# Performance work log

Hardware: AMD Instinct MI355X
Metric: run time of the kernel (lower is better)

Reference implementation:

```python
import jax, jax.numpy as jnp
import numpy as np

T, W, H = 3072, 2048, 1024   # tokens, words, hidden
C, S = 32, 3                 # labels, score channels (start/end/inside)
HID = 512                    # scorer MLP hidden
MAXW = 12                    # max span width
THR = 0.5                    # extraction threshold
N = W * MAXW                 # fixed number of enumerated spans


def setup_inputs() -> dict:
    key = jax.random.key(0)
    ks = jax.random.split(key, 16)
    hidden_states = jax.random.normal(ks[0], (T, H), jnp.float32) * 0.05
    # each word's first subword carries word_id+1; other tokens carry 0
    first_pos = (jnp.arange(W) * T // W).astype(jnp.int32)
    words_mask = jnp.zeros((T,), jnp.int32).at[first_pos].set(jnp.arange(1, W + 1, dtype=jnp.int32))
    labels_embeds = jax.random.normal(ks[1], (C, H), jnp.float32) * 0.05
    p = lambda k, shp: jax.random.normal(k, shp, jnp.float32) * 0.02
    return dict(
        hidden_states=hidden_states,
        words_mask=words_mask,
        labels_embeds=labels_embeds,
        Wt=p(ks[2], (H, 2 * H)), bt=jnp.zeros((2 * H,), jnp.float32),
        Wl=p(ks[3], (H, 2 * H)), bl=jnp.zeros((2 * H,), jnp.float32),
        W1a=p(ks[4], (H, HID)), W1b=p(ks[5], (H, HID)), W1c=p(ks[6], (H, HID)),
        b1=jnp.zeros((HID,), jnp.float32),
        W2=p(ks[7], (HID, S)), b2=jnp.zeros((S,), jnp.float32),
        Wsp1=p(ks[8], (2 * H, H)), bsp1=jnp.zeros((H,), jnp.float32),
        Wsp2=p(ks[9], (H, H)), bsp2=jnp.zeros((H,), jnp.float32),
    )


def reference(hidden_states, words_mask, labels_embeds,
              Wt, bt, Wl, bl, W1a, W1b, W1c, b1, W2, b2,
              Wsp1, bsp1, Wsp2, bsp2):
    # --- scatter token embeddings into word slots (dummy slot W absorbs mask==0) ---
    idx = jnp.where(words_mask > 0, words_mask - 1, W)
    we = jnp.zeros((W + 1, H), hidden_states.dtype).at[idx].add(hidden_states)[:W]  # [W,H]

    # --- scorer: proj to (2,H) halves, pairwise features, MLP -> [W,C,S] ---
    tok = (we @ Wt + bt).reshape(W, 2, H)
    lab = (labels_embeds @ Wl + bl).reshape(C, 2, H)
    t0, t1 = tok[:, 0], tok[:, 1]
    l0, l1 = lab[:, 0], lab[:, 1]
    # first MLP layer on concat([t0, l0, t1*l1]) computed as split matmuls
    h = (t0 @ W1a)[:, None, :] + (l0 @ W1b)[None, :, :] \
        + jnp.einsum('wh,ch,hd->wcd', t1, l1, W1c)
    h = jax.nn.relu(h + b1)
    scores = h @ W2 + b2  # [W,C,S]

    # --- threshold span extraction (fixed-shape enumeration of widths < MAXW) ---
    probs = jax.nn.sigmoid(scores)
    is_start = jnp.any(probs[..., 0] >= THR, axis=1)  # [W]
    is_end = jnp.any(probs[..., 1] >= THR, axis=1)    # [W]
    starts = jnp.repeat(jnp.arange(W), MAXW)          # [N]
    ends_raw = starts + jnp.tile(jnp.arange(MAXW), W)
    valid = ends_raw < W
    ends = jnp.minimum(ends_raw, W - 1)
    span_mask = valid & is_start[starts] & is_end[ends]  # [N]
    span_idx = jnp.stack([starts, ends], axis=-1)        # [N,2] int

    # --- span_rep_layer: gather start/end word embeds, 2-layer projection ---
    idxm = span_idx * span_mask[:, None].astype(span_idx.dtype)
    sp = jnp.concatenate([we[idxm[:, 0]], we[idxm[:, 1]]], axis=-1)  # [N,2H]
    span_rep = jax.nn.relu(sp @ Wsp1 + bsp1) @ Wsp2 + bsp2           # [N,H]

    # einsum 'BND,BCD->BNC' with B=1
    span_logits = span_rep @ labels_embeds.T  # [N,C]

    # pack_shape_prefixed_tensor equivalent: flat float payload
    flat = jnp.concatenate([
        scores.ravel(),
        span_idx.astype(scores.dtype).ravel(),
        span_mask.astype(scores.dtype),
        span_logits.ravel(),
    ])
    return flat
```

## Files before the change

kernel.cpp:

```cpp
#include <hip/hip_runtime.h>
#include <hip/hip_bf16.h>

#define W_WORDS 2048
#define H_DIM   1024
#define C_LAB   32
#define HID_D   512
#define MAXW    12
#define NSPAN   (W_WORDS * MAXW)

typedef __attribute__((ext_vector_type(8))) short bf16x8;
typedef __attribute__((ext_vector_type(4))) float f32x4;
typedef __attribute__((ext_vector_type(4))) int i32x4;
typedef __attribute__((ext_vector_type(8))) int i32x8;

__device__ __forceinline__ unsigned short f2b(float x) {
  union { float f; unsigned int i; } v; v.f = x;
  unsigned int r = v.i + 0x7FFFu + ((v.i >> 16) & 1u);
  return (unsigned short)(r >> 16);
}
__device__ __forceinline__ float b2f(unsigned short b) {
  union { float f; unsigned int i; } v; v.i = ((unsigned int)b) << 16;
  return v.f;
}

__device__ __forceinline__ unsigned char f2e4m3(float x) {
  union { float f; unsigned u; } v; v.f = x;
  unsigned sign = (v.u >> 31) << 7;
  v.u &= 0x7FFFFFFFu;
  if (v.f > 448.f) v.f = 448.f;
  int e8 = (int)(v.u >> 23) - 120;
  unsigned r;
  if (e8 >= 1) {
    unsigned m = v.u & 0x7FFFFFu;
    unsigned keep = m >> 20;
    unsigned rest = m & 0xFFFFFu;
    keep += (rest > 0x80000u) || (rest == 0x80000u && (keep & 1u));
    if (keep == 8u) { keep = 0u; ++e8; }
    if (e8 >= 16) { e8 = 15; keep = 6u; }
    else if (e8 == 15 && keep == 7u) keep = 6u;
    r = (unsigned)((e8 << 3) | keep);
  } else {
    int m = (int)(v.f * 512.f + 0.5f);
    r = (m >= 8) ? 0x08u : (unsigned)m;
  }
  return (unsigned char)(r | sign);
}

#define GLOAD_LDS16(g, l)                                                    \
  __builtin_amdgcn_global_load_lds(                                          \
      (const __attribute__((address_space(1))) unsigned int*)(g),            \
      (__attribute__((address_space(3))) unsigned int*)(l), 16, 0, 0)

__global__ void mega0_k(const float* __restrict__ hs, const int* __restrict__ wm,
    unsigned char* __restrict__ we8,
    const float* __restrict__ Wt, const float* __restrict__ W1a,
    const float* __restrict__ Wsp1, const float* __restrict__ W1c,
    const float* __restrict__ Wsp2,
    unsigned char* __restrict__ WtT8, unsigned short* __restrict__ W1aT,
    unsigned char* __restrict__ Wsp1Tc8, float* __restrict__ W1cT,
    float* __restrict__ Wsp2T, unsigned short* __restrict__ Wtb0) {
  if (blockIdx.z == 6) {
    int t = blockIdx.y * 96 + blockIdx.x;
    int m = wm[t];
    if (m <= 0) return;
    const float* src = hs + (size_t)t * H_DIM;
    unsigned char* dst = we8 + (size_t)(m - 1) * H_DIM;
    int i = (threadIdx.y * 32 + threadIdx.x) * 4;
    float4 v = *(const float4*)(src + i);
    unsigned u = (unsigned)f2e4m3(v.x * 16.f)
               | ((unsigned)f2e4m3(v.y * 16.f) << 8)
               | ((unsigned)f2e4m3(v.z * 16.f) << 16)
               | ((unsigned)f2e4m3(v.w * 16.f) << 24);
    *(unsigned*)(dst + i) = u;
    return;
  }
  int c0 = blockIdx.x * 32, r0 = blockIdx.y * 32;
  if (blockIdx.z == 7) {
    if (c0 >= 1024) return;
    for (int i = threadIdx.y; i < 32; i += 8)
      Wtb0[(size_t)(r0 + i) * 1024 + c0 + threadIdx.x] =
          f2b(Wt[(size_t)(r0 + i) * 2048 + c0 + threadIdx.x]);
    return;
  }
  const float* in;
  void* out;
  int R, C, ld, mode;
  switch (blockIdx.z) {
    case 0: in = Wt + 1024; out = WtT8; R = 1024; C = 1024; ld = 2048; mode = 2; break;
    case 1: in = W1a;  out = W1aT;   R = 1024; C = 512;  ld = 512;  mode = 1; break;
    case 2: in = Wsp1; out = Wsp1Tc8; R = 1024; C = 1024; ld = 1024; mode = 2; break;
    case 3: in = Wsp1 + 1048576; out = Wsp1Tc8 + 1048576; R = 1024; C = 1024; ld = 1024; mode = 2; break;
    case 4: in = W1c;  out = W1cT;   R = 1024; C = 512;  ld = 512;  mode = 0; break;
    default: in = Wsp2; out = Wsp2T; R = 1024; C = 1024; ld = 1024; mode = 0; break;
  }
  if (c0 >= C || r0 >= R) return;
  __shared__ float tile[32][33];
  for (int i = threadIdx.y; i < 32; i += 8)
    tile[i][threadIdx.x] = in[(size_t)(r0 + i) * ld + c0 + threadIdx.x];
  __syncthreads();
  if (mode == 2) {
    unsigned char* o = (unsigned char*)out;
    for (int i = threadIdx.y; i < 32; i += 8)
      o[(size_t)(c0 + i) * R + r0 + threadIdx.x] = f2e4m3(tile[threadIdx.x][i] * 64.f);
  } else if (mode == 1) {
    unsigned short* o = (unsigned short*)out;
    for (int i = threadIdx.y; i < 32; i += 8)
      o[(size_t)(c0 + i) * R + r0 + threadIdx.x] = f2b(tile[threadIdx.x][i]);
  } else {
    float* o = (float*)out;
    for (int i = threadIdx.y; i < 32; i += 8)
      o[(size_t)(c0 + i) * R + r0 + threadIdx.x] = tile[threadIdx.x][i];
  }
}

__device__ __forceinline__ void rgemm8_body(int N, int M,
    const float* __restrict__ A, int lda, const float* __restrict__ B, int ldb,
    const float* __restrict__ bias, float* __restrict__ out, int ldc,
    int bx, int by, float* shf) {
  float (*Asm)[1024] = (float(*)[1024])shf;
  float (*red)[16][8] = (float(*)[16][8])(shf + 8192);
  int m0 = by * 8;
  for (int idx = threadIdx.x; idx < 8 * 1024; idx += 256) {
    int mm = idx >> 10, kk = idx & 1023;
    Asm[mm][kk] = (m0 + mm < M) ? A[(size_t)(m0 + mm) * lda + kk] : 0.f;
  }
  __syncthreads();
  int tx = threadIdx.x & 15, ty = threadIdx.x >> 4;
  int n = bx * 16 + tx;
  float acc[8] = {0.f, 0.f, 0.f, 0.f, 0.f, 0.f, 0.f, 0.f};
  if (n < N) {
    for (int k = ty * 64; k < ty * 64 + 64; ++k) {
      float bv = B[(size_t)k * ldb + n];
#pragma unroll
      for (int mm = 0; mm < 8; ++mm) acc[mm] = fmaf(Asm[mm][k], bv, acc[mm]);
    }
  }
#pragma unroll
  for (int mm = 0; mm < 8; ++mm) red[ty][tx][mm] = acc[mm];
  __syncthreads();
  if (ty < 8 && n < N && m0 + ty < M) {
    float s = 0.f;
#pragma unroll
    for (int q = 0; q < 16; ++q) s += red[q][tx][ty];
    if (bias) s += bias[n];
    out[(size_t)(m0 + ty) * ldc + n] = s;
  }
}

__global__ __launch_bounds__(256) void rgemm8z_k(
    const float* __restrict__ L, const float* __restrict__ Wl,
    const float* __restrict__ bl, float* __restrict__ lab,
    const float* __restrict__ Wsp2T, float* __restrict__ MmTf) {
  __shared__ float shf[10240];
  if (blockIdx.z == 0) {
    rgemm8_body(2048, 32, L, 1024, Wl, 2048, bl, lab, 2048, blockIdx.x, blockIdx.y, shf);
  } else {
    if (blockIdx.x >= 64) return;
    rgemm8_body(1024, 32, L, 1024, Wsp2T, 1024, nullptr, MmTf, 1024,
                blockIdx.x, blockIdx.y, shf);
  }
}

__global__ __launch_bounds__(256) void mega1_k(
    const float* __restrict__ lab, const float* __restrict__ W1cT,
    unsigned char* __restrict__ KT8,
    const float* __restrict__ W1b, const float* __restrict__ b1,
    float* __restrict__ BvecB,
    const float* __restrict__ bsp2, const float* __restrict__ L,
    float* __restrict__ cv, const float* __restrict__ MmTf,
    unsigned short* __restrict__ MmTb, const float* __restrict__ W2,
    unsigned short* __restrict__ W2padT, const float* __restrict__ bsp1,
    unsigned short* __restrict__ bsp1b,
    const float* __restrict__ bt, const float* __restrict__ W1a,
    float* __restrict__ bt0A) {
  __shared__ float shf[10240];
  int g = blockIdx.x;
  if (g < 8192) {
    size_t gid = (size_t)g * 256 + threadIdx.x;
    int row = (int)(gid >> 7);
    int h0 = ((int)gid & 127) * 8;
    int c = row >> 9, d = row & 511;
    const float* lp = lab + (size_t)c * 2048 + 1024 + h0;
    const float* wp = W1cT + (size_t)d * 1024 + h0;
    float4 l0 = *(const float4*)lp, l1 = *(const float4*)(lp + 4);
    float4 w0 = *(const float4*)wp, w1 = *(const float4*)(wp + 4);
    unsigned u0 = (unsigned)f2e4m3(l0.x * w0.x * 1024.f)
                | ((unsigned)f2e4m3(l0.y * w0.y * 1024.f) << 8)
                | ((unsigned)f2e4m3(l0.z * w0.z * 1024.f) << 16)
                | ((unsigned)f2e4m3(l0.w * w0.w * 1024.f) << 24);
    unsigned u1 = (unsigned)f2e4m3(l1.x * w1.x * 1024.f)
                | ((unsigned)f2e4m3(l1.y * w1.y * 1024.f) << 8)
                | ((unsigned)f2e4m3(l1.z * w1.z * 1024.f) << 16)
                | ((unsigned)f2e4m3(l1.w * w1.w * 1024.f) << 24);
    *(uint2*)(KT8 + (size_t)row * 1024 + h0) = make_uint2(u0, u1);
  } else if (g < 8320) {
    int b = g - 8192;
    rgemm8_body(512, 32, lab, 2048, W1b, 512, b1, BvecB, 512, b & 31, b >> 5, shf);
  } else {
    int b = g - 8320;
    if (b < 32) {
      int c = b;
      float a = 0.f;
      for (int k = threadIdx.x; k < 1024; k += 256)
        a = fmaf(bsp2[k], L[(size_t)c * 1024 + k], a);
#pragma unroll
      for (int off = 32; off; off >>= 1) a += __shfl_down(a, off);
      if ((threadIdx.x & 63) == 0) shf[threadIdx.x >> 6] = a;
      __syncthreads();
      if (threadIdx.x == 0) cv[c] = shf[0] + shf[1] + shf[2] + shf[3];
    } else if (b < 64) {
      int i = (b - 32) * 1024 + threadIdx.x * 4;
      float4 v = *(const float4*)(MmTf + i);
      *(ushort4*)(MmTb + i) = make_ushort4(f2b(v.x), f2b(v.y), f2b(v.z), f2b(v.w));
    } else if (b < 96) {
      int i = (b - 64) * 256 + threadIdx.x;
      int n = i >> 9, d = i & 511;
      W2padT[i] = f2b(n < 3 ? W2[d * 3 + n] : 0.f);
    } else if (b == 96) {
      int i = threadIdx.x * 4;
      float4 v = *(const float4*)(bsp1 + i);
      *(ushort4*)(bsp1b + i) = make_ushort4(f2b(v.x), f2b(v.y), f2b(v.z), f2b(v.w));
    } else {
      float (*red)[16] = (float(*)[16])shf;
      int tx = threadIdx.x & 15, ty = threadIdx.x >> 4;
      int d = (b - 97) * 16 + tx;
      float a = 0.f;
      for (int k = ty * 64; k < ty * 64 + 64; ++k)
        a = fmaf(bt[k], W1a[(size_t)k * 512 + d], a);
      red[ty][tx] = a;
      __syncthreads();
      if (ty == 0) {
        float s = 0.f;
#pragma unroll
        for (int q = 0; q < 16; ++q) s += red[q][tx];
        bt0A[d] = s;
      }
    }
  }
}

__global__ __launch_bounds__(256) void wfuse_k(
    const unsigned short* __restrict__ A, const unsigned short* __restrict__ BT,
    unsigned char* __restrict__ out8) {
  __shared__ __align__(16) unsigned short smem[2][16384];
  int tid = threadIdx.x;
  int lane = tid & 63, wid = tid >> 6;
  int wr = wid >> 1, wc = wid & 1;
  int row0 = blockIdx.y * 128, col0 = blockIdx.x * 128;
  f32x4 zero4 = {0.f, 0.f, 0.f, 0.f};
  f32x4 acc[4][4];
#pragma unroll
  for (int i = 0; i < 4; ++i)
#pragma unroll
    for (int j = 0; j < 4; ++j) acc[i][j] = zero4;
  int srow = tid >> 3;
  int scol = ((tid & 7) ^ (srow & 7)) * 8;
  const unsigned short* gA = A + (size_t)(row0 + srow) * 1024 + scol;
  const unsigned short* gB = BT + (size_t)(col0 + srow) * 1024 + scol;
  int fr = lane & 15, hi = lane >> 4;
#define W_STAGE(buf, kt)                                                     \
  {                                                                          \
    unsigned short* dA = smem[buf] + tid * 8;                                \
    unsigned short* dB = smem[buf] + 8192 + tid * 8;                         \
    _Pragma("unroll")                                                        \
    for (int i2 = 0; i2 < 4; ++i2) {                                         \
      GLOAD_LDS16(gA + (size_t)(i2 * 32) * 1024 + (kt), dA + i2 * 2048);     \
      GLOAD_LDS16(gB + (size_t)(i2 * 32) * 1024 + (kt), dB + i2 * 2048);     \
    }                                                                        \
  }
  W_STAGE(0, 0);
  for (int t = 0; t < 16; ++t) {
    if (t + 1 < 16) {
      W_STAGE((t + 1) & 1, (t + 1) << 6);
      asm volatile("s_waitcnt vmcnt(8)" ::: "memory");
    } else {
      asm volatile("s_waitcnt vmcnt(0)" ::: "memory");
    }
    __builtin_amdgcn_sched_barrier(0);
    __builtin_amdgcn_s_barrier();
    __builtin_amdgcn_sched_barrier(0);
    const unsigned short* As = smem[t & 1];
    const unsigned short* Bs = smem[t & 1] + 8192;
    bf16x8 af[4][2], bfr[4][2];
#pragma unroll
    for (int mi = 0; mi < 4; ++mi) {
      int rl = wr * 64 + mi * 16 + fr;
#pragma unroll
      for (int kk = 0; kk < 2; ++kk)
        af[mi][kk] = *(const bf16x8*)&As[rl * 64 + (((kk << 2) | hi) ^ (rl & 7)) * 8];
    }
#pragma unroll
    for (int ni = 0; ni < 4; ++ni) {
      int rl = wc * 64 + ni * 16 + fr;
#pragma unroll
      for (int kk = 0; kk < 2; ++kk)
        bfr[ni][kk] = *(const bf16x8*)&Bs[rl * 64 + (((kk << 2) | hi) ^ (rl & 7)) * 8];
    }
#pragma unroll
    for (int kk = 0; kk < 2; ++kk)
#pragma unroll
      for (int mi = 0; mi < 4; ++mi)
#pragma unroll
        for (int ni = 0; ni < 4; ++ni)
          acc[mi][ni] = __builtin_amdgcn_mfma_f32_16x16x32_bf16(af[mi][kk], bfr[ni][kk],
                                                                acc[mi][ni], 0, 0, 0);
    __builtin_amdgcn_sched_barrier(0);
    __builtin_amdgcn_s_barrier();
  }
#undef W_STAGE
  int rbase = row0 + wr * 64 + (hi << 2);
  int cbase = col0 + wc * 64 + fr;
#pragma unroll
  for (int mi = 0; mi < 4; ++mi)
#pragma unroll
    for (int ni = 0; ni < 4; ++ni) {
      int ccol = cbase + ni * 16;
#pragma unroll
      for (int j = 0; j < 4; ++j) {
        int r = rbase + mi * 16 + j;
        out8[(size_t)r * 1024 + ccol] = f2e4m3(acc[mi][ni][j] * 64.f);
      }
    }
}

__global__ __launch_bounds__(256) void fgemm_k(
    const unsigned char* __restrict__ A, const unsigned char* __restrict__ BT,
    float* __restrict__ Avec, unsigned char* __restrict__ t1f8,
    unsigned short* __restrict__ UVb,
    const float* __restrict__ bt, const float* __restrict__ bt0A) {
  __shared__ __align__(16) unsigned char smem[2][32768];
  int tid = threadIdx.x;
  int lane = tid & 63, wid = tid >> 6;
  int wr = wid >> 1, wc = wid & 1;
  int row0 = blockIdx.y * 128, col0 = blockIdx.x * 128;
  f32x4 zero4 = {0.f, 0.f, 0.f, 0.f};
  f32x4 acc[4][4];
#pragma unroll
  for (int i = 0; i < 4; ++i)
#pragma unroll
    for (int j = 0; j < 4; ++j) acc[i][j] = zero4;
  int srow = tid >> 3;
  int s2 = (tid & 7) ^ (srow & 7);
  int scolB = (((s2 << 1) | (s2 >> 2)) & 7) * 16;
  const unsigned char* gA = A + (size_t)(row0 + srow) * 1024 + scolB;
  const unsigned char* gB = BT + (size_t)(col0 + srow) * 1024 + scolB;
  int fr = lane & 15, hi = lane >> 4;
#define F_STAGE(buf, ktB)                                                    \
  {                                                                          \
    unsigned char* dA = smem[buf] + tid * 16;                                \
    unsigned char* dB = smem[buf] + 16384 + tid * 16;                        \
    _Pragma("unroll")                                                        \
    for (int i2 = 0; i2 < 4; ++i2) {                                         \
      GLOAD_LDS16(gA + (size_t)(i2 * 32) * 1024 + (ktB), dA + i2 * 4096);    \
      GLOAD_LDS16(gB + (size_t)(i2 * 32) * 1024 + (ktB), dB + i2 * 4096);    \
    }                                                                        \
  }
  F_STAGE(0, 0);
  for (int t = 0; t < 8; ++t) {
    if (t + 1 < 8) {
      F_STAGE((t + 1) & 1, (t + 1) * 128);
      asm volatile("s_waitcnt vmcnt(8)" ::: "memory");
    } else {
      asm volatile("s_waitcnt vmcnt(0)" ::: "memory");
    }
    __builtin_amdgcn_sched_barrier(0);
    __builtin_amdgcn_s_barrier();
    __builtin_amdgcn_sched_barrier(0);
    const unsigned char* As = smem[t & 1];
    const unsigned char* Bs = smem[t & 1] + 16384;
    i32x8 af[4], bfr[4];
#pragma unroll
    for (int mi = 0; mi < 4; ++mi) {
      int rl = wr * 64 + mi * 16 + fr;
      i32x4 lo = *(const i32x4*)&As[rl * 128 + ((hi ^ (rl & 7)) * 16)];
      i32x4 h2 = *(const i32x4*)&As[rl * 128 + (((4 + hi) ^ (rl & 7)) * 16)];
      af[mi][0] = lo[0]; af[mi][1] = lo[1]; af[mi][2] = lo[2]; af[mi][3] = lo[3];
      af[mi][4] = h2[0]; af[mi][5] = h2[1]; af[mi][6] = h2[2]; af[mi][7] = h2[3];
    }
#pragma unroll
    for (int ni = 0; ni < 4; ++ni) {
      int rl = wc * 64 + ni * 16 + fr;
      i32x4 lo = *(const i32x4*)&Bs[rl * 128 + ((hi ^ (rl & 7)) * 16)];
      i32x4 h2 = *(const i32x4*)&Bs[rl * 128 + (((4 + hi) ^ (rl & 7)) * 16)];
      bfr[ni][0] = lo[0]; bfr[ni][1] = lo[1]; bfr[ni][2] = lo[2]; bfr[ni][3] = lo[3];
      bfr[ni][4] = h2[0]; bfr[ni][5] = h2[1]; bfr[ni][6] = h2[2]; bfr[ni][7] = h2[3];
    }
#pragma unroll
    for (int mi = 0; mi < 4; ++mi)
#pragma unroll
      for (int ni = 0; ni < 4; ++ni)
        acc[mi][ni] = __builtin_amdgcn_mfma_scale_f32_16x16x128_f8f6f4(
            af[mi], bfr[ni], acc[mi][ni], 0, 0, 0, 127u, 0, 127u);
    __builtin_amdgcn_sched_barrier(0);
    __builtin_amdgcn_s_barrier();
  }
#undef F_STAGE
  const float inv = 0.0009765625f;
  int rbase = row0 + wr * 64 + (hi << 2);
  int cbase = col0 + wc * 64 + fr;
#pragma unroll
  for (int mi = 0; mi < 4; ++mi)
#pragma unroll
    for (int ni = 0; ni < 4; ++ni) {
      int ccol = cbase + ni * 16;
#pragma unroll
      for (int j = 0; j < 4; ++j) {
        int r = rbase + mi * 16 + j;
        float v = acc[mi][ni][j] * inv;
        if (ccol < 1024) {
          t1f8[(size_t)r * 1024 + ccol] = f2e4m3((v + bt[1024 + ccol]) * 16.f);
        } else if (ccol < 3072) {
          UVb[(size_t)r * 2048 + (ccol - 1024)] = f2b(v);
        } else {
          Avec[(size_t)r * 512 + (ccol - 3072)] = v + bt0A[ccol - 3072];
        }
      }
    }
}

__global__ __launch_bounds__(256) void egemm_k(
    const unsigned char* __restrict__ A,
    const unsigned char* __restrict__ BT,
    const float* __restrict__ avec, const float* __restrict__ bvec,
    const unsigned short* __restrict__ w2t, float* __restrict__ sPart) {
  __shared__ __align__(16) unsigned char smem[2][32768];
  int tid = threadIdx.x;
  int lane = tid & 63, wid = tid >> 6;
  int wr = wid >> 1, wc = wid & 1;
  int bid = blockIdx.x;
  int xcd = bid & 7, ii = bid >> 3;
  int sg = ii >> 6, inner = ii & 63;
  int rb = ((sg >> 1) << 3) | (inner & 7);
  int cb = xcd * 16 + (((sg & 1) << 3) | (inner >> 3));
  int row0 = rb * 128, col0 = cb * 128, cbq = cb & 3;

  f32x4 zero4 = {0.f, 0.f, 0.f, 0.f};
  f32x4 acc[4][4];
#pragma unroll
  for (int i = 0; i < 4; ++i)
#pragma unroll
    for (int j = 0; j < 4; ++j) acc[i][j] = zero4;

  int srow = tid >> 3;
  int s2 = (tid & 7) ^ (srow & 7);
  int scolB = (((s2 << 1) | (s2 >> 2)) & 7) * 16;
  const unsigned char* gA = A + (size_t)(row0 + srow) * 1024 + scolB;
  const unsigned char* gB = BT + (size_t)(col0 + srow) * 1024 + scolB;

  int fr = lane & 15, hi = lane >> 4;

#define E_STAGE(buf, ktB)                                                    \
  {                                                                          \
    unsigned char* dA = smem[buf] + tid * 16;                                \
    unsigned char* dB = smem[buf] + 16384 + tid * 16;                        \
    _Pragma("unroll")                                                        \
    for (int i2 = 0; i2 < 4; ++i2) {                                         \
      GLOAD_LDS16(gA + (size_t)(i2 * 32) * 1024 + (ktB), dA + i2 * 4096);    \
      GLOAD_LDS16(gB + (size_t)(i2 * 32) * 1024 + (ktB), dB + i2 * 4096);    \
    }                                                                        \
  }

  E_STAGE(0, 0);

  for (int t = 0; t < 8; ++t) {
    if (t + 1 < 8) {
      E_STAGE((t + 1) & 1, (t + 1) * 128);
      asm volatile("s_waitcnt vmcnt(8)" ::: "memory");
    } else {
      asm volatile("s_waitcnt vmcnt(0)" ::: "memory");
    }
    __builtin_amdgcn_sched_barrier(0);
    __builtin_amdgcn_s_barrier();
    __builtin_amdgcn_sched_barrier(0);

    const unsigned char* As = smem[t & 1];
    const unsigned char* Bs = smem[t & 1] + 16384;
    i32x8 af[4], bfr[4];
#pragma unroll
    for (int mi = 0; mi < 4; ++mi) {
      int rl = wr * 64 + mi * 16 + fr;
      i32x4 lo = *(const i32x4*)&As[rl * 128 + ((hi ^ (rl & 7)) * 16)];
      i32x4 h2 = *(const i32x4*)&As[rl * 128 + (((4 + hi) ^ (rl & 7)) * 16)];
      af[mi][0] = lo[0]; af[mi][1] = lo[1]; af[mi][2] = lo[2]; af[mi][3] = lo[3];
      af[mi][4] = h2[0]; af[mi][5] = h2[1]; af[mi][6] = h2[2]; af[mi][7] = h2[3];
    }
#pragma unroll
    for (int ni = 0; ni < 4; ++ni) {
      int rl = wc * 64 + ni * 16 + fr;
      i32x4 lo = *(const i32x4*)&Bs[rl * 128 + ((hi ^ (rl & 7)) * 16)];
      i32x4 h2 = *(const i32x4*)&Bs[rl * 128 + (((4 + hi) ^ (rl & 7)) * 16)];
      bfr[ni][0] = lo[0]; bfr[ni][1] = lo[1]; bfr[ni][2] = lo[2]; bfr[ni][3] = lo[3];
      bfr[ni][4] = h2[0]; bfr[ni][5] = h2[1]; bfr[ni][6] = h2[2]; bfr[ni][7] = h2[3];
    }
#pragma unroll
    for (int mi = 0; mi < 4; ++mi)
#pragma unroll
      for (int ni = 0; ni < 4; ++ni)
        acc[mi][ni] = __builtin_amdgcn_mfma_scale_f32_16x16x128_f8f6f4(
            af[mi], bfr[ni], acc[mi][ni], 0, 0, 0, 127u, 0, 127u);
    __builtin_amdgcn_sched_barrier(0);
    __builtin_amdgcn_s_barrier();
  }
#undef E_STAGE

  unsigned short* hsm = (unsigned short*)&smem[0][0];
  int cc = col0 >> 9;
  int dg0 = col0 & 511;
  const float inv = 6.103515625e-05f;
#pragma unroll
  for (int mi = 0; mi < 4; ++mi) {
#pragma unroll
    for (int j = 0; j < 4; ++j) {
      int rl = wr * 64 + hi * 4 + mi * 16 + j;
      const float* avp = avec + (size_t)(row0 + rl) * 512 + dg0;
      const float* bvp = bvec + (size_t)cc * 512 + dg0;
#pragma unroll
      for (int ni = 0; ni < 4; ++ni) {
        int cl = wc * 64 + ni * 16 + fr;
        float v = acc[mi][ni][j] * inv + avp[cl] + bvp[cl];
        v = fmaxf(v, 0.f);
        int slot = cl >> 3;
        hsm[rl * 128 + (((slot ^ rl) & 7) << 3) + (slot & 8) * 8 + (cl & 7)] = f2b(v);
      }
    }
  }
  __syncthreads();
  f32x4 s0 = zero4, s1 = zero4;
  int r0l = wid * 32 + fr;
  int r1l = wid * 32 + 16 + fr;
#pragma unroll
  for (int kt2 = 0; kt2 < 4; ++kt2) {
    int slot = kt2 * 4 + hi;
    bf16x8 a0 = *(const bf16x8*)&hsm[r0l * 128 + (((slot ^ r0l) & 7) << 3) + (slot & 8) * 8];
    bf16x8 a1 = *(const bf16x8*)&hsm[r1l * 128 + (((slot ^ r1l) & 7) << 3) + (slot & 8) * 8];
    bf16x8 b = *(const bf16x8*)&w2t[(size_t)fr * 512 + dg0 + kt2 * 32 + hi * 8];
    s0 = __builtin_amdgcn_mfma_f32_16x16x32_bf16(a0, b, s0, 0, 0, 0);
    s1 = __builtin_amdgcn_mfma_f32_16x16x32_bf16(a1, b, s1, 0, 0, 0);
  }
  if (fr < 3) {
    float* sp = sPart + ((size_t)cbq * 2048 + row0) * 96 + cc * 3 + fr;
#pragma unroll
    for (int j = 0; j < 4; ++j) {
      sp[(size_t)(wid * 32 + hi * 4 + j) * 96] = s0[j];
      sp[(size_t)(wid * 32 + 16 + hi * 4 + j) * 96] = s1[j];
    }
  }
}

__global__ __launch_bounds__(256) void foldmask_k(const float* __restrict__ part,
    const float* __restrict__ b2, float* __restrict__ outS,
    int* __restrict__ is_s, int* __restrict__ is_e) {
  __shared__ float sc[192];
  int b = blockIdx.x;
  int i = threadIdx.x;
  if (i < 192) {
    int idx = b * 192 + i;
    float s = b2[i % 3] + part[idx] + part[196608 + idx] +
              part[2 * 196608 + idx] + part[3 * 196608 + idx];
    outS[idx] = s;
    sc[i] = s;
  }
  __syncthreads();
  if (i < 2) {
    int s = 0, e = 0;
#pragma unroll
    for (int c = 0; c < 32; ++c) {
      s |= (sc[i * 96 + c * 3 + 0] >= 0.f);
      e |= (sc[i * 96 + c * 3 + 1] >= 0.f);
    }
    is_s[2 * b + i] = s;
    is_e[2 * b + i] = e;
  }
}

__global__ __launch_bounds__(256) void spanfuse_k(
    const unsigned short* __restrict__ UVb, const unsigned short* __restrict__ bsp1b,
    const unsigned short* __restrict__ MmTb, const float* __restrict__ cvv,
    const int* __restrict__ is_s, const int* __restrict__ is_e,
    float* __restrict__ outIdx, float* __restrict__ outMask,
    float* __restrict__ outLog) {
  __shared__ __align__(16) unsigned short Rs[4][2][16][32];
  int tid = threadIdx.x, lane = tid & 63, w = tid >> 6;
  int fr = lane & 15, hi = lane >> 4;
  int row = lane >> 2, q = lane & 3;
  int n = blockIdx.x * 64 + w * 16 + row;
  int wi = n / MAXW;
  int j = n - wi * MAXW;
  int er = wi + j;
  int valid = er < W_WORDS;
  int e = valid ? er : (W_WORDS - 1);
  int mask = (valid && is_s[wi] && is_e[e]) ? 1 : 0;
  if (q == 0) {
    outIdx[2 * n] = (float)wi;
    outIdx[2 * n + 1] = (float)e;
    outMask[n] = (float)mask;
  }
  int si = mask ? wi : 0, ei = mask ? e : 0;
  const unsigned short* Up = UVb + (size_t)si * 2048 + q * 8;
  const unsigned short* Vp = UVb + (size_t)ei * 2048 + 1024 + q * 8;
  const unsigned short* bp = bsp1b + q * 8;
  const unsigned short* M0 = MmTb + (size_t)fr * 1024 + hi * 8;
  const unsigned short* M1 = MmTb + (size_t)(16 + fr) * 1024 + hi * 8;
  unsigned short* wRs0 = &Rs[w][0][0][0];
  unsigned short* wRs1 = &Rs[w][1][0][0];
  int wslot = (q ^ (row & 3)) * 8;
  int rslot = ((hi ^ (fr & 3)) & 3) * 8;
  f32x4 zero4 = {0.f, 0.f, 0.f, 0.f};
  f32x4 a0 = zero4, a1 = zero4;

  bf16x8 u0 = *(const bf16x8*)Up,        v0 = *(const bf16x8*)Vp;
  bf16x8 b0 = *(const bf16x8*)bp;
  bf16x8 u1 = *(const bf16x8*)(Up + 32), v1 = *(const bf16x8*)(Vp + 32);
  bf16x8 b1v = *(const bf16x8*)(bp + 32);
  bf16x8 f00 = *(const bf16x8*)M0,        f10 = *(const bf16x8*)M1;
  bf16x8 f01 = *(const bf16x8*)(M0 + 32), f11 = *(const bf16x8*)(M1 + 32);

  for (int kt = 0; kt < 32; kt += 2) {
    int ka = ((kt + 2) & 31) * 32, kb = ((kt + 3) & 31) * 32;
    bf16x8 nu0 = *(const bf16x8*)(Up + ka), nv0 = *(const bf16x8*)(Vp + ka);
    bf16x8 nb0 = *(const bf16x8*)(bp + ka);
    bf16x8 nu1 = *(const bf16x8*)(Up + kb), nv1 = *(const bf16x8*)(Vp + kb);
    bf16x8 nb1 = *(const bf16x8*)(bp + kb);
    bf16x8 nf00 = *(const bf16x8*)(M0 + ka), nf10 = *(const bf16x8*)(M1 + ka);
    bf16x8 nf01 = *(const bf16x8*)(M0 + kb), nf11 = *(const bf16x8*)(M1 + kb);

    bf16x8 o0, o1;
#pragma unroll
    for (int i = 0; i < 8; ++i) {
      o0[i] = (short)f2b(fmaxf(b2f((unsigned short)u0[i]) + b2f((unsigned short)v0[i]) +
                               b2f((unsigned short)b0[i]), 0.f));
      o1[i] = (short)f2b(fmaxf(b2f((unsigned short)u1[i]) + b2f((unsigned short)v1[i]) +
                               b2f((unsigned short)b1v[i]), 0.f));
    }
    *(bf16x8*)&wRs0[row * 32 + wslot] = o0;
    *(bf16x8*)&wRs1[row * 32 + wslot] = o1;
    asm volatile("s_waitcnt lgkmcnt(0)" ::: "memory");
    bf16x8 fa0 = *(const bf16x8*)&wRs0[fr * 32 + rslot];
    bf16x8 fa1 = *(const bf16x8*)&wRs1[fr * 32 + rslot];
    a0 = __builtin_amdgcn_mfma_f32_16x16x32_bf16(fa0, f00, a0, 0, 0, 0);
    a1 = __builtin_amdgcn_mfma_f32_16x16x32_bf16(fa0, f10, a1, 0, 0, 0);
    a0 = __builtin_amdgcn_mfma_f32_16x16x32_bf16(fa1, f01, a0, 0, 0, 0);
    a1 = __builtin_amdgcn_mfma_f32_16x16x32_bf16(fa1, f11, a1, 0, 0, 0);
    u0 = nu0; v0 = nv0; b0 = nb0;
    u1 = nu1; v1 = nv1; b1v = nb1;
    f00 = nf00; f10 = nf10; f01 = nf01; f11 = nf11;
  }

  int n0 = blockIdx.x * 64 + w * 16;
  float c0 = cvv[fr], c1 = cvv[16 + fr];
#pragma unroll
  for (int jj = 0; jj < 4; ++jj) {
    int nn = n0 + hi * 4 + jj;
    outLog[(size_t)nn * 32 + fr] = a0[jj] + c0;
    outLog[(size_t)nn * 32 + 16 + fr] = a1[jj] + c1;
  }
}

extern "C" void kernel_launch(void* const* d_in, const int* in_sizes, int n_in,
                              void* d_out, int out_size, void* d_ws, size_t ws_size,
                              hipStream_t stream) {
  const float* hs   = (const float*)d_in[0];
  const int*   wm   = (const int*)d_in[1];
  const float* L    = (const float*)d_in[2];
  const float* Wt   = (const float*)d_in[3];
  const float* bt   = (const float*)d_in[4];
  const float* Wl   = (const float*)d_in[5];
  const float* bl   = (const float*)d_in[6];
  const float* W1a  = (const float*)d_in[7];
  const float* W1b  = (const float*)d_in[8];
  const float* W1c  = (const float*)d_in[9];
  const float* b1   = (const float*)d_in[10];
  const float* W2   = (const float*)d_in[11];
  const float* b2   = (const float*)d_in[12];
  const float* Wsp1 = (const float*)d_in[13];
  const float* bsp1 = (const float*)d_in[14];
  const float* Wsp2 = (const float*)d_in[15];
  const float* bsp2 = (const float*)d_in[16];

  char* p = (char*)d_ws;
  auto alloc = [&p](size_t bytes) {
    char* r = p;
    p += (bytes + 255) & ~(size_t)255;
    return r;
  };
  unsigned char*  we8    = (unsigned char*)alloc((size_t)2048 * 1024);
  unsigned char*  WtT8    = (unsigned char*)alloc((size_t)1024 * 1024);
  unsigned char*  Wsp1Tc8 = (unsigned char*)alloc((size_t)2048 * 1024);
  unsigned char*  WfuseT8 = (unsigned char*)alloc((size_t)512 * 1024);
  unsigned char*  t1f8   = (unsigned char*)alloc((size_t)2048 * 1024);
  float*          lab    = (float*)alloc((size_t)32 * 2048 * 4);
  unsigned short* W1aT   = (unsigned short*)alloc((size_t)512 * 1024 * 2);
  unsigned short* Wtb0   = (unsigned short*)alloc((size_t)1024 * 1024 * 2);
  float*          Avec   = (float*)alloc((size_t)2048 * 512 * 4);
  float*          BvecB  = (float*)alloc((size_t)32 * 512 * 4);
  float*          bt0A   = (float*)alloc(512 * 4);
  float*          W1cT   = (float*)alloc((size_t)512 * 1024 * 4);
  unsigned char*  KT8    = (unsigned char*)alloc((size_t)16384 * 1024);
  float*          sPart  = (float*)alloc((size_t)4 * 2048 * 96 * 4);
  int*            is_s   = (int*)alloc(2048 * 4);
  int*            is_e   = (int*)alloc(2048 * 4);
  unsigned short* UVb    = (unsigned short*)alloc((size_t)2048 * 2048 * 2);
  float*          Wsp2T  = (float*)alloc((size_t)1024 * 1024 * 4);
  float*          MmTf   = (float*)alloc((size_t)32 * 1024 * 4);
  unsigned short* MmTb   = (unsigned short*)alloc((size_t)32 * 1024 * 2);
  float*          cv     = (float*)alloc(32 * 4);
  unsigned short* W2padT = (unsigned short*)alloc((size_t)16 * 512 * 2);
  unsigned short* bsp1b  = (unsigned short*)alloc((size_t)1024 * 2);

  float* outS    = (float*)d_out;
  float* outIdx  = outS + (size_t)2048 * 32 * 3;
  float* outMask = outIdx + (size_t)NSPAN * 2;
  float* outLog  = outMask + NSPAN;

  mega0_k<<<dim3(96, 32, 8), dim3(32, 8), 0, stream>>>(
      hs, wm, we8, Wt, W1a, Wsp1, W1c, Wsp2, WtT8, W1aT, Wsp1Tc8, W1cT, Wsp2T, Wtb0);

  rgemm8z_k<<<dim3(128, 4, 2), 256, 0, stream>>>(L, Wl, bl, lab, Wsp2T, MmTf);

  mega1_k<<<8449, 256, 0, stream>>>(lab, W1cT, KT8, W1b, b1, BvecB,
                                    bsp2, L, cv, MmTf, MmTb, W2, W2padT, bsp1, bsp1b,
                                    bt, W1a, bt0A);

  wfuse_k<<<dim3(8, 4), 256, 0, stream>>>(W1aT, Wtb0, WfuseT8);

  fgemm_k<<<dim3(28, 16), 256, 0, stream>>>(we8, WtT8, Avec, t1f8, UVb, bt, bt0A);

  egemm_k<<<2048, 256, 0, stream>>>(t1f8, KT8, Avec, BvecB, W2padT, sPart);

  foldmask_k<<<1024, 256, 0, stream>>>(sPart, b2, outS, is_s, is_e);

  spanfuse_k<<<384, 256, 0, stream>>>(UVb, bsp1b, MmTb, cv, is_s, is_e,
                                      outIdx, outMask, outLog);
}
```

Measured before the change: 191.7 us.

## Fold wfuse GEMM into mega1 launch and remap egemm block tile order

The standalone wfuse_k GEMM (32 blocks) now runs as extra blocks appended to the mega1_k grid, which removes one kernel launch and lets that small GEMM overlap with mega1's elementwise work. Because of this, mega1's shared memory grows from 40KB to 64KB for every block, which may cut occupancy for the 8192 lightweight elementwise blocks. Separately, egemm_k's block-to-tile mapping changes so each XCD walks row blocks in pairs of adjacent column tiles, altering L2 reuse.

Measured after the change: 194.9 us. No clear change (+1.6%).

```diff
diff --git a/kernel.cpp b/kernel.cpp
--- a/kernel.cpp
+++ b/kernel.cpp
@@ -172,8 +172,11 @@
     unsigned short* __restrict__ W2padT, const float* __restrict__ bsp1,
     unsigned short* __restrict__ bsp1b,
     const float* __restrict__ bt, const float* __restrict__ W1a,
-    float* __restrict__ bt0A) {
-  __shared__ float shf[10240];
+    float* __restrict__ bt0A,
+    const unsigned short* __restrict__ W1aT, const unsigned short* __restrict__ Wtb0,
+    unsigned char* __restrict__ WfuseT8) {
+  __shared__ __align__(16) unsigned char shraw[65536];
+  float* shf = (float*)shraw;
   int g = blockIdx.x;
   if (g < 8192) {
     size_t gid = (size_t)g * 256 + threadIdx.x;
@@ -196,7 +199,7 @@
   } else if (g < 8320) {
     int b = g - 8192;
     rgemm8_body(512, 32, lab, 2048, W1b, 512, b1, BvecB, 512, b & 31, b >> 5, shf);
-  } else {
+  } else if (g < 8449) {
     int b = g - 8320;
     if (b < 32) {
       int c = b;
@@ -236,91 +239,89 @@
         bt0A[d] = s;
       }
     }
-  }
-}
-
-__global__ __launch_bounds__(256) void wfuse_k(
-    const unsigned short* __restrict__ A, const unsigned short* __restrict__ BT,
-    unsigned char* __restrict__ out8) {
-  __shared__ __align__(16) unsigned short smem[2][16384];
-  int tid = threadIdx.x;
-  int lane = tid & 63, wid = tid >> 6;
-  int wr = wid >> 1, wc = wid & 1;
-  int row0 = blockIdx.y * 128, col0 = blockIdx.x * 128;
-  f32x4 zero4 = {0.f, 0.f, 0.f, 0.f};
-  f32x4 acc[4][4];
-#pragma unroll
-  for (int i = 0; i < 4; ++i)
-#pragma unroll
-    for (int j = 0; j < 4; ++j) acc[i][j] = zero4;
-  int srow = tid >> 3;
-  int scol = ((tid & 7) ^ (srow & 7)) * 8;
-  const unsigned short* gA = A + (size_t)(row0 + srow) * 1024 + scol;
-  const unsigned short* gB = BT + (size_t)(col0 + srow) * 1024 + scol;
-  int fr = lane & 15, hi = lane >> 4;
+  } else {
+    int idx = g - 8449;
+    int row0 = (idx >> 3) * 128, col0 = (idx & 7) * 128;
+    int tid = threadIdx.x;
+    int lane = tid & 63, wid = tid >> 6;
+    int wr = wid >> 1, wc = wid & 1;
+    f32x4 zero4 = {0.f, 0.f, 0.f, 0.f};
+    f32x4 acc[4][4];
+#pragma unroll
+    for (int i = 0; i < 4; ++i)
+#pragma unroll
+      for (int j = 0; j < 4; ++j) acc[i][j] = zero4;
+    int srow = tid >> 3;
+    int scol = ((tid & 7) ^ (srow & 7)) * 8;
+    const unsigned short* gA = W1aT + (size_t)(row0 + srow) * 1024 + scol;
+    const unsigned short* gB = Wtb0 + (size_t)(col0 + srow) * 1024 + scol;
+    int fr = lane & 15, hi = lane >> 4;
+#define WF_SM(buf) ((unsigned short*)shraw + (buf) * 16384)
 #define W_STAGE(buf, kt)                                                     \
-  {                                                                          \
-    unsigned short* dA = smem[buf] + tid * 8;                                \
-    unsigned short* dB = smem[buf] + 8192 + tid * 8;                         \
-    _Pragma("unroll")                                                        \
-    for (int i2 = 0; i2 < 4; ++i2) {                                         \
-      GLOAD_LDS16(gA + (size_t)(i2 * 32) * 1024 + (kt), dA + i2 * 2048);     \
-      GLOAD_LDS16(gB + (size_t)(i2 * 32) * 1024 + (kt), dB + i2 * 2048);     \
-    }                                                                        \
-  }
-  W_STAGE(0, 0);
-  for (int t = 0; t < 16; ++t) {
-    if (t + 1 < 16) {
-      W_STAGE((t + 1) & 1, (t + 1) << 6);
-      asm volatile("s_waitcnt vmcnt(8)" ::: "memory");
-    } else {
-      asm volatile("s_waitcnt vmcnt(0)" ::: "memory");
-    }
-    __builtin_amdgcn_sched_barrier(0);
-    __builtin_amdgcn_s_barrier();
-    __builtin_amdgcn_sched_barrier(0);
-    const unsigned short* As = smem[t & 1];
-    const unsigned short* Bs = smem[t & 1] + 8192;
-    bf16x8 af[4][2], bfr[4][2];
-#pragma unroll
-    for (int mi = 0; mi < 4; ++mi) {
-      int rl = wr * 64 + mi * 16 + fr;
+    {                                                                        \
+      unsigned short* dA = WF_SM(buf) + tid * 8;                             \
+      unsigned short* dB = WF_SM(buf) + 8192 + tid * 8;                      \
+      _Pragma("unroll")                                                      \
+      for (int i2 = 0; i2 < 4; ++i2) {                                       \
+        GLOAD_LDS16(gA + (size_t)(i2 * 32) * 1024 + (kt), dA + i2 * 2048);   \
+        GLOAD_LDS16(gB + (size_t)(i2 * 32) * 1024 + (kt), dB + i2 * 2048);   \
+      }                                                                      \
+    }
+    W_STAGE(0, 0);
+    for (int t = 0; t < 16; ++t) {
+      if (t + 1 < 16) {
+        W_STAGE((t + 1) & 1, (t + 1) << 6);
+        asm volatile("s_waitcnt vmcnt(8)" ::: "memory");
+      } else {
+        asm volatile("s_waitcnt vmcnt(0)" ::: "memory");
+      }
+      __builtin_amdgcn_sched_barrier(0);
+      __builtin_amdgcn_s_barrier();
+      __builtin_amdgcn_sched_barrier(0);
+      const unsigned short* As = WF_SM(t & 1);
+      const unsigned short* Bs = As + 8192;
+      bf16x8 af[4][2], bfr[4][2];
+#pragma unroll
+      for (int mi = 0; mi < 4; ++mi) {
+        int rl = wr * 64 + mi * 16 + fr;
+#pragma unroll
+        for (int kk = 0; kk < 2; ++kk)
+          af[mi][kk] = *(const bf16x8*)&As[rl * 64 + (((kk << 2) | hi) ^ (rl & 7)) * 8];
+      }
+#pragma unroll
+      for (int ni = 0; ni < 4; ++ni) {
+        int rl = wc * 64 + ni * 16 + fr;
+#pragma unroll
+        for (int kk = 0; kk < 2; ++kk)
+          bfr[ni][kk] = *(const bf16x8*)&Bs[rl * 64 + (((kk << 2) | hi) ^ (rl & 7)) * 8];
+      }
 #pragma unroll
       for (int kk = 0; kk < 2; ++kk)
-        af[mi][kk] = *(const bf16x8*)&As[rl * 64 + (((kk << 2) | hi) ^ (rl & 7)) * 8];
-    }
-#pragma unroll
-    for (int ni = 0; ni < 4; ++ni) {
-      int rl = wc * 64 + ni * 16 + fr;
-#pragma unroll
-      for (int kk = 0; kk < 2; ++kk)
-        bfr[ni][kk] = *(const bf16x8*)&Bs[rl * 64 + (((kk << 2) | hi) ^ (rl & 7)) * 8];
-    }
-#pragma unroll
-    for (int kk = 0; kk < 2; ++kk)
-#pragma unroll
-      for (int mi = 0; mi < 4; ++mi)
-#pragma unroll
-        for (int ni = 0; ni < 4; ++ni)
-          acc[mi][ni] = __builtin_amdgcn_mfma_f32_16x16x32_bf16(af[mi][kk], bfr[ni][kk],
-                                                                acc[mi][ni], 0, 0, 0);
-    __builtin_amdgcn_sched_barrier(0);
-    __builtin_amdgcn_s_barrier();
-  }
+#pragma unroll
+        for (int mi = 0; mi < 4; ++mi)
+#pragma unroll
+          for (int ni = 0; ni < 4; ++ni)
+            acc[mi][ni] = __builtin_amdgcn_mfma_f32_16x16x32_bf16(af[mi][kk], bfr[ni][kk],
+                                                                  acc[mi][ni], 0, 0, 0);
+      __builtin_amdgcn_sched_barrier(0);
+      __builtin_amdgcn_s_barrier();
+    }
 #undef W_STAGE
-  int rbase = row0 + wr * 64 + (hi << 2);
-  int cbase = col0 + wc * 64 + fr;
-#pragma unroll
-  for (int mi = 0; mi < 4; ++mi)
-#pragma unroll
-    for (int ni = 0; ni < 4; ++ni) {
-      int ccol = cbase + ni * 16;
-#pragma unroll
-      for (int j = 0; j < 4; ++j) {
-        int r = rbase + mi * 16 + j;
-        out8[(size_t)r * 1024 + ccol] = f2e4m3(acc[mi][ni][j] * 64.f);
+#undef WF_SM
+    int rbase = row0 + wr * 64 + (hi << 2);
+    int cbase = col0 + wc * 64 + fr;
+#pragma unroll
+    for (int mi = 0; mi < 4; ++mi)
+#pragma unroll
+      for (int ni = 0; ni < 4; ++ni) {
+        int ccol = cbase + ni * 16;
+#pragma unroll
+        for (int j = 0; j < 4; ++j) {
+          int r = rbase + mi * 16 + j;
+          WfuseT8[(size_t)r * 1024 + ccol] = f2e4m3(acc[mi][ni][j] * 64.f);
+        }
       }
-    }
+  }
 }
 
 __global__ __launch_bounds__(256) void fgemm_k(
@@ -429,9 +430,10 @@
   int wr = wid >> 1, wc = wid & 1;
   int bid = blockIdx.x;
   int xcd = bid & 7, ii = bid >> 3;
-  int sg = ii >> 6, inner = ii & 63;
-  int rb = ((sg >> 1) << 3) | (inner & 7);
-  int cb = xcd * 16 + (((sg & 1) << 3) | (inner >> 3));
+  int cbp = ii >> 5;
+  int inner = ii & 31;
+  int rb = inner >> 1;
+  int cb = xcd * 16 + cbp * 2 + (inner & 1);
   int row0 = rb * 128, col0 = cb * 128, cbq = cb & 3;
 
   f32x4 zero4 = {0.f, 0.f, 0.f, 0.f};
@@ -717,11 +719,9 @@
 
   rgemm8z_k<<<dim3(128, 4, 2), 256, 0, stream>>>(L, Wl, bl, lab, Wsp2T, MmTf);
 
-  mega1_k<<<8449, 256, 0, stream>>>(lab, W1cT, KT8, W1b, b1, BvecB,
+  mega1_k<<<8481, 256, 0, stream>>>(lab, W1cT, KT8, W1b, b1, BvecB,
                                     bsp2, L, cv, MmTf, MmTb, W2, W2padT, bsp1, bsp1b,
-                                    bt, W1a, bt0A);
-
-  wfuse_k<<<dim3(8, 4), 256, 0, stream>>>(W1aT, Wtb0, WfuseT8);
+                                    bt, W1a, bt0A, W1aT, Wtb0, WfuseT8);
 
   fgemm_k<<<dim3(28, 16), 256, 0, stream>>>(we8, WtT8, Avec, t1f8, UVb, bt, bt0A);
 
```
